# Optimization experiments

Hardware: AMD Instinct MI355X
Metric: run time of the kernel (lower is better)

Reference implementation:

```python
import jax, jax.numpy as jnp
import numpy as np

B, T, D, H, W = 4, 4096, 1024, 16, 64  # batch, seq, dim, heads, window_size
HD = D // H
NW = T // W  # num_windows (T divisible by W -> pad=0)


def setup_inputs() -> dict:
    key = jax.random.key(0)
    ks = jax.random.split(key, 7)
    x = jax.random.normal(ks[0], (B, T, D), dtype=jnp.float32)
    W_qkv = jax.random.normal(ks[1], (3 * D, D), dtype=jnp.float32) * 0.02
    W_out = jax.random.normal(ks[2], (D, D), dtype=jnp.float32) * 0.02
    b_out = jnp.zeros((D,), dtype=jnp.float32)
    W_cross = jax.random.normal(ks[3], (D, D), dtype=jnp.float32) * 0.02
    b_cross = jnp.zeros((D,), dtype=jnp.float32)
    jitter = jax.random.permutation(ks[4], NW)  # fixed permutation (stands in for torch.randperm)
    return {"x": x, "W_qkv": W_qkv, "W_out": W_out, "b_out": b_out,
            "W_cross": W_cross, "b_cross": b_cross, "jitter": jitter}


def reference(x, W_qkv, W_out, b_out, W_cross, b_cross, jitter):
    scale = HD ** -0.5
    # qkv projection (no bias)
    qkv = x @ W_qkv.T                      # (B,T,3D)
    q, k, v = jnp.split(qkv, 3, axis=-1)

    def to_windows(t):  # (B,T,D) -> (B,H,NW,W,HD)
        return t.reshape(B, T, H, HD).transpose(0, 2, 1, 3).reshape(B, H, NW, W, HD)

    q_w, k_w, v_w = to_windows(q), to_windows(k), to_windows(v)

    # local windowed attention
    attn = jnp.einsum('bhnqd,bhnkd->bhnqk', q_w, k_w) * scale
    attn = jax.nn.softmax(attn, axis=-1)
    local = jnp.einsum('bhnqk,bhnkd->bhnqd', attn, v_w)      # (B,H,NW,W,HD)
    local = local.reshape(B, H, T, HD).transpose(0, 2, 1, 3).reshape(B, T, D)

    # cross-window summary exchange
    scores = jnp.tanh(x @ W_cross.T + b_cross).mean(-1)       # (B,T)
    weights = jax.nn.softmax(scores.reshape(B, NW, W), axis=-1)
    summaries = jnp.einsum('bnw,bnwd->bnd', weights, x.reshape(B, NW, W, D))  # (B,NW,D)
    jittered = summaries[:, jitter, :]
    cs_attn = jax.nn.softmax(jnp.einsum('bnd,bmd->bnm', summaries, jittered) * (D ** -0.5), axis=-1)
    cs_out = jnp.einsum('bnm,bmd->bnd', cs_attn, jittered)    # (B,NW,D)
    cs_exp = jnp.broadcast_to(cs_out[:, :, None, :], (B, NW, W, D)).reshape(B, T, D)

    final = local + 0.25 * cs_exp
    return final @ W_out.T + b_out
```

## Files before the change

kernel.cpp:

```cpp
#include <hip/hip_runtime.h>

typedef unsigned short u16;
typedef float f32x4 __attribute__((ext_vector_type(4)));
typedef __bf16 bf16x8 __attribute__((ext_vector_type(8)));

#define T_ 4096
#define D_ 1024
#define NW_ 64

__device__ __forceinline__ float b2f(u16 u) {
  return __uint_as_float(((unsigned)u) << 16);
}
__device__ __forceinline__ u16 f2bf(float f) {
  unsigned u = __float_as_uint(f);
  u += 0x7fffu + ((u >> 16) & 1u);
  return (u16)(u >> 16);
}
__device__ __forceinline__ void g2l16(const u16* g, u16* l) {
  __builtin_amdgcn_global_load_lds((const __attribute__((address_space(1))) void*)g,
                                   (__attribute__((address_space(3))) void*)l, 16, 0, 0);
}

__global__ __launch_bounds__(256) void cvt3_k(const float* __restrict__ s0, u16* __restrict__ d0,
                                              const float* __restrict__ s1, u16* __restrict__ d1,
                                              const float* __restrict__ s2, u16* __restrict__ d2)
{
  long bid = blockIdx.x;
  const float* src; u16* dst; long base;
  if (bid < 16384)      { src = s0; dst = d0; base = bid * 1024; }
  else if (bid < 19456) { src = s1; dst = d1; base = (bid - 16384) * 1024; }
  else                  { src = s2; dst = d2; base = (bid - 19456) * 1024; }
  long i = base + (long)threadIdx.x * 4;
  float4 v = *(const float4*)(src + i);
  ushort4 o;
  o.x = f2bf(v.x); o.y = f2bf(v.y); o.z = f2bf(v.z); o.w = f2bf(v.w);
  *(ushort4*)(dst + i) = o;
}

__global__ __launch_bounds__(256) void cvt_k(const float* __restrict__ src,
                                             u16* __restrict__ dst, long n)
{
  long i = ((long)blockIdx.x * 256 + threadIdx.x) * 4;
  if (i >= n) return;
  float4 v = *(const float4*)(src + i);
  ushort4 o;
  o.x = f2bf(v.x); o.y = f2bf(v.y); o.z = f2bf(v.z); o.w = f2bf(v.w);
  *(ushort4*)(dst + i) = o;
}

__global__ __launch_bounds__(512, 2) void gemm256(
    const u16* __restrict__ A, const u16* __restrict__ Bm,
    u16* __restrict__ C16, float* __restrict__ C32,
    const float* __restrict__ bias, int M, int N, int K, int lda)
{
  __shared__ u16 AS[2][2][8192];
  __shared__ u16 BS[2][2][8192];
  (void)M;
  const int tid = threadIdx.x;
  const int lane = tid & 63;
  const int w = tid >> 6;
  const int wm = w >> 2, wn = w & 3;
  const int q = lane >> 4, il = lane & 15;

  const int nbx = gridDim.x;
  const int nwg = nbx * (int)gridDim.y;
  const int bid = (int)blockIdx.y * nbx + (int)blockIdx.x;
  const int nid = (bid & 7) * (nwg >> 3) + (bid >> 3);
  const long m0 = (long)(nid / nbx) * 256;
  const long n0 = (long)(nid % nbx) * 256;

  const int nt = K >> 6;

  const int u0 = tid, u1 = 512 + tid;
  const int r0 = u0 >> 3, r1 = u1 >> 3;
  const int sx0 = ((u0 & 7) ^ (r0 & 7)) << 3;
  const int sx1 = ((u1 & 7) ^ (r1 & 7)) << 3;
  const long gar0 = m0 + (r0 >> 6) * 128 + (r0 & 63);
  const long gar1 = m0 + (r1 >> 6) * 128 + (r1 & 63);
  const long gbr0 = n0 + (r0 >> 5) * 64 + (r0 & 31);
  const long gbr1 = n0 + (r1 >> 5) * 64 + (r1 & 31);
  const int dl = w * 512;

  const int aro = (wm * 64 + il) * 64;
  const int bro = (wn * 32 + il) * 64;
  const int ax = (il & 7) << 3;
  const int ko0 = (q * 8) ^ ax;
  const int ko1 = (32 + q * 8) ^ ax;

  f32x4 acc[8][4] = {};
  bf16x8 af[4][2], bf0[2][2], bf1[2][2];

#define STGA(BUF, MH, KT) do { \
    g2l16(A + (gar0 + (MH) * 64) * (long)lda + (KT) * 64 + sx0, &AS[BUF][MH][dl]); \
    g2l16(A + (gar1 + (MH) * 64) * (long)lda + (KT) * 64 + sx1, &AS[BUF][MH][4096 + dl]); \
  } while (0)
#define STGB(BUF, NH, KT) do { \
    g2l16(Bm + (gbr0 + (NH) * 32) * (long)K + (KT) * 64 + sx0, &BS[BUF][NH][dl]); \
    g2l16(Bm + (gbr1 + (NH) * 32) * (long)K + (KT) * 64 + sx1, &BS[BUF][NH][4096 + dl]); \
  } while (0)
#define LDAF(BUF, MH) do { \
    _Pragma("unroll") for (int f = 0; f < 4; ++f) { \
      af[f][0] = *(const bf16x8*)&AS[BUF][MH][aro + f * 1024 + ko0]; \
      af[f][1] = *(const bf16x8*)&AS[BUF][MH][aro + f * 1024 + ko1]; \
    } } while (0)
#define LDBF(BUF, NH, BF) do { \
    _Pragma("unroll") for (int j = 0; j < 2; ++j) { \
      BF[j][0] = *(const bf16x8*)&BS[BUF][NH][bro + j * 1024 + ko0]; \
      BF[j][1] = *(const bf16x8*)&BS[BUF][NH][bro + j * 1024 + ko1]; \
    } } while (0)
#define MFMAQ(MH, NH, BF) do { \
    _Pragma("unroll") for (int f = 0; f < 4; ++f) { \
      _Pragma("unroll") for (int j = 0; j < 2; ++j) { \
        acc[(MH)*4+f][(NH)*2+j] = __builtin_amdgcn_mfma_f32_16x16x32_bf16(af[f][0], BF[j][0], acc[(MH)*4+f][(NH)*2+j], 0, 0, 0); \
        acc[(MH)*4+f][(NH)*2+j] = __builtin_amdgcn_mfma_f32_16x16x32_bf16(af[f][1], BF[j][1], acc[(MH)*4+f][(NH)*2+j], 0, 0, 0); \
      } } } while (0)
#define BARR() __builtin_amdgcn_s_barrier()
#define WL0() asm volatile("s_waitcnt lgkmcnt(0)" ::: "memory")
#define WV8() asm volatile("s_waitcnt vmcnt(8)" ::: "memory")
#define CFENCE() asm volatile("" ::: "memory")
#define PRIO(x) __builtin_amdgcn_s_setprio(x)

  STGA(0, 0, 0);
  STGB(0, 0, 0);
  STGB(0, 1, 0);
  STGA(0, 1, 0);
  STGA(1, 0, 1);
  STGB(1, 0, 1);
  WV8();
  BARR();

  for (int tt = 0; tt < nt; tt += 2) {
    const int k1 = tt + 1;
    const int k2 = tt + 2 < nt ? tt + 2 : nt - 1;
    const int k3 = tt + 3 < nt ? tt + 3 : nt - 1;
    LDAF(0, 0); LDBF(0, 0, bf0);
    STGB(1, 1, k1);
    BARR(); WL0();
    PRIO(1); MFMAQ(0, 0, bf0); PRIO(0);
    WV8(); BARR();
    LDBF(0, 1, bf1);
    STGA(1, 1, k1);
    BARR(); WL0();
    PRIO(1); MFMAQ(0, 1, bf1); PRIO(0);
    WV8(); BARR();
    LDAF(0, 1);
    STGA(0, 0, k2);
    BARR(); WL0();
    PRIO(1); MFMAQ(1, 0, bf0); PRIO(0);
    BARR(); CFENCE();
    STGB(0, 0, k2);
    BARR();
    PRIO(1); MFMAQ(1, 1, bf1); PRIO(0);
    WV8(); BARR();
    LDAF(1, 0); LDBF(1, 0, bf0);
    STGB(0, 1, k2);
    BARR(); WL0();
    PRIO(1); MFMAQ(0, 0, bf0); PRIO(0);
    WV8(); BARR();
    LDBF(1, 1, bf1);
    STGA(0, 1, k2);
    BARR(); WL0();
    PRIO(1); MFMAQ(0, 1, bf1); PRIO(0);
    WV8(); BARR();
    LDAF(1, 1);
    STGA(1, 0, k3);
    BARR(); WL0();
    PRIO(1); MFMAQ(1, 0, bf0); PRIO(0);
    BARR(); CFENCE();
    STGB(1, 0, k3);
    BARR();
    PRIO(1); MFMAQ(1, 1, bf1); PRIO(0);
    WV8(); BARR();
  }

  asm volatile("s_waitcnt vmcnt(0)" ::: "memory");

#pragma unroll
  for (int ni = 0; ni < 4; ++ni) {
    const long col = n0 + wn * 64 + ni * 16 + il;
    const float bv = bias ? bias[col] : 0.0f;
#pragma unroll
    for (int mi = 0; mi < 8; ++mi) {
#pragma unroll
      for (int r = 0; r < 4; ++r) {
        const long row = m0 + wm * 128 + (mi >> 2) * 64 + (mi & 3) * 16 + q * 4 + r;
        const float v = acc[mi][ni][r] + bv;
        if (C32) C32[row * N + col] = v;
        else     C16[row * N + col] = f2bf(v);
      }
    }
  }
#undef STGA
#undef STGB
#undef LDAF
#undef LDBF
#undef MFMAQ
#undef BARR
#undef WL0
#undef WV8
#undef CFENCE
#undef PRIO
}

__global__ __launch_bounds__(256) void scores_k(const u16* __restrict__ y,
                                                float* __restrict__ scores)
{
  const int lane = threadIdx.x & 63;
  const long r = (long)blockIdx.x * 4 + (threadIdx.x >> 6);
  const u16* p = y + r * D_ + lane * 16;
  uint4 v0 = *(const uint4*)p;
  uint4 v1 = *(const uint4*)(p + 8);
  union { uint4 v; u16 s[8]; } a, c;
  a.v = v0; c.v = v1;
  float s = 0.f;
#pragma unroll
  for (int e = 0; e < 8; ++e) s += tanhf(b2f(a.s[e]));
#pragma unroll
  for (int e = 0; e < 8; ++e) s += tanhf(b2f(c.s[e]));
#pragma unroll
  for (int o = 32; o; o >>= 1) s += __shfl_xor(s, o, 64);
  if (lane == 0) scores[r] = s * (1.0f / 1024.0f);
}

__global__ __launch_bounds__(256) void summar_k(const float* __restrict__ x,
                                                const float* __restrict__ scores,
                                                float* __restrict__ summ)
{
  __shared__ float wts[64];
  const int tid = threadIdx.x;
  const int b = blockIdx.x >> 6, n = blockIdx.x & 63;
  if (tid < 64) {
    float v = scores[(long)b * T_ + n * 64 + tid];
    float mx = v;
#pragma unroll
    for (int o = 32; o; o >>= 1) mx = fmaxf(mx, __shfl_xor(mx, o, 64));
    float e = __expf(v - mx);
    float s = e;
#pragma unroll
    for (int o = 32; o; o >>= 1) s += __shfl_xor(s, o, 64);
    wts[tid] = e / s;
  }
  __syncthreads();
  const int d0 = tid * 4;
  const float* xp = x + ((long)b * T_ + n * 64) * D_ + d0;
  float a0 = 0, a1 = 0, a2 = 0, a3 = 0;
#pragma unroll 4
  for (int wd = 0; wd < 64; ++wd) {
    float4 v = *(const float4*)(xp + (long)wd * D_);
    float wv = wts[wd];
    a0 += wv * v.x; a1 += wv * v.y; a2 += wv * v.z; a3 += wv * v.w;
  }
  *(float4*)(summ + ((long)b * NW_ + n) * D_ + d0) = make_float4(a0, a1, a2, a3);
}

__global__ __launch_bounds__(256) void cross_k(const float* __restrict__ summ,
                                               const int* __restrict__ jitter,
                                               float* __restrict__ cso)
{
  __shared__ float sm[64], pm[64];
  __shared__ int jidx[64];
  const int tid = threadIdx.x;
  const int b = blockIdx.x >> 6, n = blockIdx.x & 63;
  if (tid < 64) jidx[tid] = jitter[tid];
  __syncthreads();
  const int m = tid >> 2, part = tid & 3;
  const float* sn = summ + ((long)b * NW_ + n) * D_;
  const float* sj = summ + ((long)b * NW_ + jidx[m]) * D_;
  float p = 0.f;
  for (int d = part * 256; d < part * 256 + 256; d += 4) {
    float4 aa = *(const float4*)(sn + d);
    float4 bb = *(const float4*)(sj + d);
    p += aa.x * bb.x + aa.y * bb.y + aa.z * bb.z + aa.w * bb.w;
  }
  p += __shfl_xor(p, 1, 64);
  p += __shfl_xor(p, 2, 64);
  if (part == 0) sm[m] = p * (1.0f / 32.0f);
  __syncthreads();
  if (tid < 64) {
    float v = sm[tid], mx = v;
#pragma unroll
    for (int o = 32; o; o >>= 1) mx = fmaxf(mx, __shfl_xor(mx, o, 64));
    float e = __expf(v - mx), s = e;
#pragma unroll
    for (int o = 32; o; o >>= 1) s += __shfl_xor(s, o, 64);
    pm[tid] = e / s;
  }
  __syncthreads();
  const int d0 = tid * 4;
  float a0 = 0, a1 = 0, a2 = 0, a3 = 0;
  for (int mm = 0; mm < 64; ++mm) {
    const float* sr = summ + ((long)b * NW_ + jidx[mm]) * D_ + d0;
    float wv = pm[mm];
    float4 vv = *(const float4*)sr;
    a0 += wv * vv.x; a1 += wv * vv.y; a2 += wv * vv.z; a3 += wv * vv.w;
  }
  *(float4*)(cso + ((long)b * NW_ + n) * D_ + d0) = make_float4(a0, a1, a2, a3);
}

__global__ __launch_bounds__(256) void attn_win(u16* qkv,
                                                const float* __restrict__ cso)
{
  __shared__ u16 Qs[64 * 72], Ks[64 * 72], Vt[64 * 72], Ps[64 * 72];
  unsigned* Vt32 = (unsigned*)Vt;
  const int tid = threadIdx.x;
  const int lane = tid & 63;
  const int w = tid >> 6;
  const int q = lane >> 4, il = lane & 15;
  const int bid = blockIdx.x;
  const int n = bid & 63;
  const int h = (bid >> 6) & 15;
  const int b = bid >> 10;
  const long rowbase = (long)b * T_ + n * 64;

#pragma unroll
  for (int i = 0; i < 2; ++i) {
    int u = i * 256 + tid;
    int row = u >> 3, cp = u & 7;
    const u16* src = qkv + (rowbase + row) * 3072 + h * 64 + cp * 8;
    uint4 qv = *(const uint4*)src;
    uint4 kv = *(const uint4*)(src + 1024);
    uint4 vv = *(const uint4*)(src + 2048);
    *(uint4*)&Qs[row * 72 + cp * 8] = qv;
    *(uint4*)&Ks[row * 72 + cp * 8] = kv;
    union { uint4 v; unsigned u[4]; } mine, part;
    mine.v = vv;
#pragma unroll
    for (int m = 0; m < 4; ++m) part.u[m] = __shfl_xor(mine.u[m], 8, 64);
    const bool even = ((row & 1) == 0);
    const int p = row >> 1;
#pragma unroll
    for (int m = 0; m < 4; ++m) {
      unsigned word = even ? ((mine.u[m] & 0xffffu) | (part.u[m] << 16))
                           : ((part.u[m] >> 16)     | (mine.u[m] & 0xffff0000u));
      int c = cp * 8 + 2 * m + (even ? 0 : 1);
      Vt32[c * 36 + p] = word;
    }
  }
  __syncthreads();

  f32x4 sacc[4] = {};
#pragma unroll
  for (int ks = 0; ks < 2; ++ks) {
    bf16x8 aq = *(const bf16x8*)&Qs[(w * 16 + il) * 72 + ks * 32 + q * 8];
#pragma unroll
    for (int ct = 0; ct < 4; ++ct) {
      bf16x8 bk = *(const bf16x8*)&Ks[(ct * 16 + il) * 72 + ks * 32 + q * 8];
      sacc[ct] = __builtin_amdgcn_mfma_f32_16x16x32_bf16(aq, bk, sacc[ct], 0, 0, 0);
    }
  }

#pragma unroll
  for (int r = 0; r < 4; ++r) {
    float s0 = sacc[0][r] * 0.125f, s1 = sacc[1][r] * 0.125f,
          s2 = sacc[2][r] * 0.125f, s3 = sacc[3][r] * 0.125f;
    float mx = fmaxf(fmaxf(s0, s1), fmaxf(s2, s3));
#pragma unroll
    for (int o = 1; o < 16; o <<= 1) mx = fmaxf(mx, __shfl_xor(mx, o, 64));
    float e0 = __expf(s0 - mx), e1 = __expf(s1 - mx),
          e2 = __expf(s2 - mx), e3 = __expf(s3 - mx);
    float sum = e0 + e1 + e2 + e3;
#pragma unroll
    for (int o = 1; o < 16; o <<= 1) sum += __shfl_xor(sum, o, 64);
    float inv = 1.0f / sum;
    int prow = w * 16 + q * 4 + r;
    Ps[prow * 72 + 0 * 16 + il] = f2bf(e0 * inv);
    Ps[prow * 72 + 1 * 16 + il] = f2bf(e1 * inv);
    Ps[prow * 72 + 2 * 16 + il] = f2bf(e2 * inv);
    Ps[prow * 72 + 3 * 16 + il] = f2bf(e3 * inv);
  }
  __syncthreads();

  f32x4 oacc[4] = {};
#pragma unroll
  for (int ks = 0; ks < 2; ++ks) {
    bf16x8 ap = *(const bf16x8*)&Ps[(w * 16 + il) * 72 + ks * 32 + q * 8];
#pragma unroll
    for (int dt = 0; dt < 4; ++dt) {
      bf16x8 bv = *(const bf16x8*)&Vt[(dt * 16 + il) * 72 + ks * 32 + q * 8];
      oacc[dt] = __builtin_amdgcn_mfma_f32_16x16x32_bf16(ap, bv, oacc[dt], 0, 0, 0);
    }
  }

  const float* cs = cso + ((long)b * NW_ + n) * D_ + h * 64;
#pragma unroll
  for (int dt = 0; dt < 4; ++dt) {
    int col = dt * 16 + il;
    float cadd = 0.25f * cs[col];
#pragma unroll
    for (int r = 0; r < 4; ++r) {
      int row = w * 16 + q * 4 + r;
      qkv[(rowbase + row) * 3072 + h * 64 + col] = f2bf(oacc[dt][r] + cadd);
    }
  }
}

extern "C" void kernel_launch(void* const* d_in, const int* in_sizes, int n_in,
                              void* d_out, int out_size, void* d_ws, size_t ws_size,
                              hipStream_t stream)
{
  (void)in_sizes; (void)n_in; (void)out_size; (void)ws_size;
  const float* x      = (const float*)d_in[0];
  const float* Wqkv   = (const float*)d_in[1];
  const float* Wout   = (const float*)d_in[2];
  const float* bout   = (const float*)d_in[3];
  const float* Wcross = (const float*)d_in[4];
  const float* bcross = (const float*)d_in[5];
  const int*   jitter = (const int*)d_in[6];
  float* out = (float*)d_out;

  char* ws = (char*)d_ws;
  u16*   qkv    = (u16*)ws;
  u16*   y      = (u16*)ws;
  u16*   xb     = (u16*)(ws + 100663296);
  u16*   wqkvb  = (u16*)(ws + 134217728);
  u16*   wtmp   = (u16*)(ws + 140509184);
  float* scores = (float*)(ws + 142606336);
  float* summ   = (float*)(ws + 142671872);
  float* cso    = (float*)(ws + 143720448);

  dim3 blk(256);
  dim3 gblk(512);
  cvt3_k<<<20480, blk, 0, stream>>>(x, xb, Wqkv, wqkvb, Wcross, wtmp);
  gemm256<<<dim3(4, 64), gblk, 0, stream>>>(xb, wtmp, y, nullptr, bcross, 16384, 1024, 1024, 1024);
  cvt_k<<<1024, blk, 0, stream>>>(Wout, wtmp, 1048576L);
  scores_k<<<4096, blk, 0, stream>>>(y, scores);
  summar_k<<<256, blk, 0, stream>>>(x, scores, summ);
  cross_k<<<256, blk, 0, stream>>>(summ, jitter, cso);
  gemm256<<<dim3(12, 64), gblk, 0, stream>>>(xb, wqkvb, qkv, nullptr, nullptr, 16384, 3072, 1024, 1024);
  attn_win<<<4096, blk, 0, stream>>>(qkv, cso);
  gemm256<<<dim3(4, 64), gblk, 0, stream>>>(qkv, wtmp, nullptr, out, bout, 16384, 1024, 1024, 3072);
}
```

Measured before the change: 419.3 us.

## Stage GEMM epilogue through swizzled LDS and deepen prefetch schedule

The GEMM epilogue now writes accumulators into shared memory with an XOR swizzle, then reads them back as 16-byte vectors so global stores are wide and coalesced instead of scattered scalar writes. The fp32 path does this in two halves to fit in LDS. The k-loop prefetch order is also reshuffled so one more stage is in flight, with vmcnt(6) waits placed less often. This adds extra barriers and an LDS round trip in the epilogue, and the new wait placement must still be correct.

```diff
diff --git a/kernel.cpp b/kernel.cpp
--- a/kernel.cpp
+++ b/kernel.cpp
@@ -53,8 +53,7 @@
     u16* __restrict__ C16, float* __restrict__ C32,
     const float* __restrict__ bias, int M, int N, int K, int lda)
 {
-  __shared__ u16 AS[2][2][8192];
-  __shared__ u16 BS[2][2][8192];
+  __shared__ u16 SH[65536];
   (void)M;
   const int tid = threadIdx.x;
   const int lane = tid & 63;
@@ -70,6 +69,7 @@
   const long n0 = (long)(nid % nbx) * 256;
 
   const int nt = K >> 6;
+  const int ntm1 = nt - 1;
 
   const int u0 = tid, u1 = 512 + tid;
   const int r0 = u0 >> 3, r1 = u1 >> 3;
@@ -90,23 +90,25 @@
   f32x4 acc[8][4] = {};
   bf16x8 af[4][2], bf0[2][2], bf1[2][2];
 
+#define ASP(BUF, MH) (&SH[((BUF) * 2 + (MH)) * 8192])
+#define BSP(BUF, NH) (&SH[32768 + ((BUF) * 2 + (NH)) * 8192])
 #define STGA(BUF, MH, KT) do { \
-    g2l16(A + (gar0 + (MH) * 64) * (long)lda + (KT) * 64 + sx0, &AS[BUF][MH][dl]); \
-    g2l16(A + (gar1 + (MH) * 64) * (long)lda + (KT) * 64 + sx1, &AS[BUF][MH][4096 + dl]); \
+    g2l16(A + (gar0 + (MH) * 64) * (long)lda + (KT) * 64 + sx0, ASP(BUF, MH) + dl); \
+    g2l16(A + (gar1 + (MH) * 64) * (long)lda + (KT) * 64 + sx1, ASP(BUF, MH) + 4096 + dl); \
   } while (0)
 #define STGB(BUF, NH, KT) do { \
-    g2l16(Bm + (gbr0 + (NH) * 32) * (long)K + (KT) * 64 + sx0, &BS[BUF][NH][dl]); \
-    g2l16(Bm + (gbr1 + (NH) * 32) * (long)K + (KT) * 64 + sx1, &BS[BUF][NH][4096 + dl]); \
+    g2l16(Bm + (gbr0 + (NH) * 32) * (long)K + (KT) * 64 + sx0, BSP(BUF, NH) + dl); \
+    g2l16(Bm + (gbr1 + (NH) * 32) * (long)K + (KT) * 64 + sx1, BSP(BUF, NH) + 4096 + dl); \
   } while (0)
 #define LDAF(BUF, MH) do { \
     _Pragma("unroll") for (int f = 0; f < 4; ++f) { \
-      af[f][0] = *(const bf16x8*)&AS[BUF][MH][aro + f * 1024 + ko0]; \
-      af[f][1] = *(const bf16x8*)&AS[BUF][MH][aro + f * 1024 + ko1]; \
+      af[f][0] = *(const bf16x8*)(ASP(BUF, MH) + aro + f * 1024 + ko0); \
+      af[f][1] = *(const bf16x8*)(ASP(BUF, MH) + aro + f * 1024 + ko1); \
     } } while (0)
 #define LDBF(BUF, NH, BF) do { \
     _Pragma("unroll") for (int j = 0; j < 2; ++j) { \
-      BF[j][0] = *(const bf16x8*)&BS[BUF][NH][bro + j * 1024 + ko0]; \
-      BF[j][1] = *(const bf16x8*)&BS[BUF][NH][bro + j * 1024 + ko1]; \
+      BF[j][0] = *(const bf16x8*)(BSP(BUF, NH) + bro + j * 1024 + ko0); \
+      BF[j][1] = *(const bf16x8*)(BSP(BUF, NH) + bro + j * 1024 + ko1); \
     } } while (0)
 #define MFMAQ(MH, NH, BF) do { \
     _Pragma("unroll") for (int f = 0; f < 4; ++f) { \
@@ -116,80 +118,120 @@
       } } } while (0)
 #define BARR() __builtin_amdgcn_s_barrier()
 #define WL0() asm volatile("s_waitcnt lgkmcnt(0)" ::: "memory")
-#define WV8() asm volatile("s_waitcnt vmcnt(8)" ::: "memory")
-#define CFENCE() asm volatile("" ::: "memory")
+#define WV6() asm volatile("s_waitcnt vmcnt(6)" ::: "memory")
 #define PRIO(x) __builtin_amdgcn_s_setprio(x)
 
-  STGA(0, 0, 0);
-  STGB(0, 0, 0);
-  STGB(0, 1, 0);
-  STGA(0, 1, 0);
-  STGA(1, 0, 1);
-  STGB(1, 0, 1);
-  WV8();
+  STGA(0, 0, 0); STGB(0, 0, 0); STGB(0, 1, 0); STGA(0, 1, 0);
+  STGA(1, 0, 1); STGB(1, 0, 1); STGB(1, 1, 1);
+  WV6();
   BARR();
 
   for (int tt = 0; tt < nt; tt += 2) {
-    const int k1 = tt + 1;
-    const int k2 = tt + 2 < nt ? tt + 2 : nt - 1;
-    const int k3 = tt + 3 < nt ? tt + 3 : nt - 1;
+    const int t1 = tt + 1;
+    const int t2 = tt + 2 <= ntm1 ? tt + 2 : ntm1;
+    const int t3 = tt + 3 <= ntm1 ? tt + 3 : ntm1;
     LDAF(0, 0); LDBF(0, 0, bf0);
-    STGB(1, 1, k1);
+    STGA(1, 1, t1);
     BARR(); WL0();
     PRIO(1); MFMAQ(0, 0, bf0); PRIO(0);
-    WV8(); BARR();
+    BARR();
     LDBF(0, 1, bf1);
-    STGA(1, 1, k1);
+    STGA(0, 0, t2);
     BARR(); WL0();
     PRIO(1); MFMAQ(0, 1, bf1); PRIO(0);
-    WV8(); BARR();
+    BARR();
     LDAF(0, 1);
-    STGA(0, 0, k2);
+    STGB(0, 0, t2);
     BARR(); WL0();
     PRIO(1); MFMAQ(1, 0, bf0); PRIO(0);
-    BARR(); CFENCE();
-    STGB(0, 0, k2);
+    BARR();
+    STGB(0, 1, t2);
     BARR();
     PRIO(1); MFMAQ(1, 1, bf1); PRIO(0);
-    WV8(); BARR();
+    WV6(); BARR();
     LDAF(1, 0); LDBF(1, 0, bf0);
-    STGB(0, 1, k2);
+    STGA(0, 1, t2);
     BARR(); WL0();
     PRIO(1); MFMAQ(0, 0, bf0); PRIO(0);
-    WV8(); BARR();
+    BARR();
     LDBF(1, 1, bf1);
-    STGA(0, 1, k2);
+    STGA(1, 0, t3);
     BARR(); WL0();
     PRIO(1); MFMAQ(0, 1, bf1); PRIO(0);
-    WV8(); BARR();
+    BARR();
     LDAF(1, 1);
-    STGA(1, 0, k3);
+    STGB(1, 0, t3);
     BARR(); WL0();
     PRIO(1); MFMAQ(1, 0, bf0); PRIO(0);
-    BARR(); CFENCE();
-    STGB(1, 0, k3);
+    BARR();
+    STGB(1, 1, t3);
     BARR();
     PRIO(1); MFMAQ(1, 1, bf1); PRIO(0);
-    WV8(); BARR();
+    WV6(); BARR();
   }
 
   asm volatile("s_waitcnt vmcnt(0)" ::: "memory");
-
-#pragma unroll
-  for (int ni = 0; ni < 4; ++ni) {
-    const long col = n0 + wn * 64 + ni * 16 + il;
-    const float bv = bias ? bias[col] : 0.0f;
-#pragma unroll
-    for (int mi = 0; mi < 8; ++mi) {
-#pragma unroll
-      for (int r = 0; r < 4; ++r) {
-        const long row = m0 + wm * 128 + (mi >> 2) * 64 + (mi & 3) * 16 + q * 4 + r;
-        const float v = acc[mi][ni][r] + bv;
-        if (C32) C32[row * N + col] = v;
-        else     C16[row * N + col] = f2bf(v);
+  __syncthreads();
+
+  if (C32) {
+    float* Cf = (float*)SH;
+#pragma unroll
+    for (int h = 0; h < 2; ++h) {
+      if (wm == h) {
+#pragma unroll
+        for (int ni = 0; ni < 4; ++ni) {
+          const int ccol = wn * 64 + ni * 16 + il;
+          const float bv = bias ? bias[n0 + ccol] : 0.0f;
+#pragma unroll
+          for (int mi = 0; mi < 8; ++mi) {
+#pragma unroll
+            for (int r = 0; r < 4; ++r) {
+              const int crow = (mi >> 2) * 64 + (mi & 3) * 16 + q * 4 + r;
+              const int byte = (crow * 1024 + ccol * 4) ^ (((crow >> 2) & 1) << 6);
+              *(float*)((char*)Cf + byte) = acc[mi][ni][r] + bv;
+            }
+          }
+        }
       }
-    }
-  }
+      __syncthreads();
+#pragma unroll
+      for (int i = 0; i < 16; ++i) {
+        const int u = i * 512 + tid;
+        const int crow = u >> 6, c16 = u & 63;
+        const int byte = (crow * 1024 + c16 * 16) ^ (((crow >> 2) & 1) << 6);
+        float4 v = *(const float4*)((char*)Cf + byte);
+        *(float4*)(C32 + (m0 + h * 128 + crow) * N + n0 + c16 * 4) = v;
+      }
+      __syncthreads();
+    }
+  } else {
+    u16* Cs = (u16*)SH;
+#pragma unroll
+    for (int ni = 0; ni < 4; ++ni) {
+      const int ccol = wn * 64 + ni * 16 + il;
+      const float bv = bias ? bias[n0 + ccol] : 0.0f;
+#pragma unroll
+      for (int mi = 0; mi < 8; ++mi) {
+#pragma unroll
+        for (int r = 0; r < 4; ++r) {
+          const int crow = wm * 128 + (mi >> 2) * 64 + (mi & 3) * 16 + q * 4 + r;
+          const int byte = (crow * 512 + ccol * 2) ^ (((crow >> 2) & 3) << 5);
+          *(u16*)((char*)Cs + byte) = f2bf(acc[mi][ni][r] + bv);
+        }
+      }
+    }
+    __syncthreads();
+#pragma unroll
+    for (int i = 0; i < 16; ++i) {
+      const int u = i * 512 + tid;
+      const int crow = u >> 5, c16 = u & 31;
+      const int byte = (crow * 512 + c16 * 16) ^ (((crow >> 2) & 3) << 5);
+      uint4 v = *(const uint4*)((char*)Cs + byte);
+      *(uint4*)(C16 + (m0 + crow) * N + n0 + c16 * 8) = v;
+    }
+  }
+#undef ASP
+#undef BSP
 #undef STGA
 #undef STGB
 #undef LDAF
@@ -197,8 +239,7 @@
 #undef MFMAQ
 #undef BARR
 #undef WL0
-#undef WV8
-#undef CFENCE
+#undef WV6
 #undef PRIO
 }
 
```

After: 379.0 us. -9.6%, faster.
